# Kernel optimization log

Hardware: AMD Instinct MI355X
Metric: run time of the kernel (lower is better)

The kernel has to match this reference:

```python
import jax, jax.numpy as jnp
import numpy as np

N_NODES = 100000
N_EDGES = 1600000
IN_F = 128
HID = 64
N_CLASSES = 2


def gcn_conv(x, W, b, src, dst, dinv, n):
    # x: [N, Fin]; W: [Fin, Fout]; src/dst: [E'] (with self-loops); dinv: [N]
    h = x @ W                                    # [N, Fout]
    norm = dinv[src] * dinv[dst]                 # [E'] symmetric normalization
    msg = h[src] * norm[:, None]                 # gather + scale, [E', Fout]
    out = jax.ops.segment_sum(msg, dst, num_segments=n)  # scatter-add, [N, Fout]
    return out + b


def setup_inputs() -> dict:
    key = jax.random.key(0)
    k1, k2, k3, k4 = jax.random.split(key, 4)
    x = jax.random.normal(k1, (N_NODES, IN_F), dtype=jnp.float32)
    edge_index = jax.random.randint(k2, (2, N_EDGES), 0, N_NODES, dtype=jnp.int64)
    W1 = jax.random.normal(k3, (IN_F, HID), dtype=jnp.float32) * (1.0 / np.sqrt(IN_F))
    b1 = jnp.zeros((HID,), dtype=jnp.float32)
    W2 = jax.random.normal(k4, (HID, N_CLASSES), dtype=jnp.float32) * (1.0 / np.sqrt(HID))
    b2 = jnp.zeros((N_CLASSES,), dtype=jnp.float32)
    return {"x": x, "edge_index": edge_index, "W1": W1, "b1": b1, "W2": W2, "b2": b2}


def reference(x, edge_index, W1, b1, W2, b2):
    n = x.shape[0]
    # add self-loops (PyG GCNConv default add_self_loops=True)
    loops = jnp.arange(n, dtype=edge_index.dtype)
    src = jnp.concatenate([edge_index[0], loops])
    dst = jnp.concatenate([edge_index[1], loops])
    # degrees on dst (with self-loops) -> D^{-1/2}; deg >= 1 so no div-by-zero
    deg = jax.ops.segment_sum(jnp.ones_like(dst, dtype=x.dtype), dst, num_segments=n)
    dinv = jax.lax.rsqrt(deg)
    h = gcn_conv(x, W1, b1, src, dst, dinv, n)
    h = jax.nn.relu(h)
    # dropout p=0.5 only in training mode; reference runs eval -> identity
    out = gcn_conv(h, W2, b2, src, dst, dinv, n)
    return out
```

## Files before the change

kernel.cpp:

```cpp
#include <hip/hip_runtime.h>
#include <hip/hip_fp16.h>

#define N_NODES 100000
#define N_EDGES 1600000
#define IN_F 128
#define HID 64
#define NBUCK 1563
#define NBP 1600
#define GS 512

typedef _Float16 half8 __attribute__((ext_vector_type(8)));
typedef _Float16 half4v __attribute__((ext_vector_type(4)));
typedef _Float16 half2v __attribute__((ext_vector_type(2)));
typedef float f32x4 __attribute__((ext_vector_type(4)));

__global__ __launch_bounds__(256) void k_hist_g(const int* __restrict__ dst,
                                                unsigned short* __restrict__ gcnt) {
    __shared__ int h[NBP];
    for (int t = threadIdx.x; t < NBP; t += 256) h[t] = 0;
    __syncthreads();
    const int g = blockIdx.x;
    const int NQ = N_EDGES / 4;
    const int4* dst4 = (const int4*)dst;
    for (int q = g * 256 + threadIdx.x; q < NQ; q += GS * 256) {
        int4 d4 = dst4[q];
        atomicAdd(&h[d4.x >> 6], 1);
        atomicAdd(&h[d4.y >> 6], 1);
        atomicAdd(&h[d4.z >> 6], 1);
        atomicAdd(&h[d4.w >> 6], 1);
    }
    __syncthreads();
    unsigned int* row = (unsigned int*)(gcnt + g * NBP);
    for (int t = threadIdx.x; t < NBP / 2; t += 256)
        row[t] = (unsigned)h[2 * t] | ((unsigned)h[2 * t + 1] << 16);
}

__global__ __launch_bounds__(512) void k_gbase(const unsigned short* __restrict__ gcnt,
                                               unsigned short* __restrict__ pre,
                                               int* __restrict__ bt) {
    __shared__ uint4 s[512];
    const int t = threadIdx.x;
    const int b0 = blockIdx.x * 8;
    const int g = ((t & 63) << 3) | (t >> 6);
    uint4 v = *(const uint4*)(gcnt + g * NBP + b0);
    uint4 run = v;
    s[t] = run;
    __syncthreads();
    for (int o = 1; o < 512; o <<= 1) {
        uint4 tt = {0u, 0u, 0u, 0u};
        if (t >= o) tt = s[t - o];
        __syncthreads();
        run.x += tt.x; run.y += tt.y; run.z += tt.z; run.w += tt.w;
        s[t] = run;
        __syncthreads();
    }
    uint4 ex = { run.x - v.x, run.y - v.y, run.z - v.z, run.w - v.w };
    *(uint4*)(pre + g * NBP + b0) = ex;
    if (t == 511) {
        bt[b0 + 0] = run.x & 0xFFFF; bt[b0 + 1] = run.x >> 16;
        bt[b0 + 2] = run.y & 0xFFFF; bt[b0 + 3] = run.y >> 16;
        bt[b0 + 4] = run.z & 0xFFFF; bt[b0 + 5] = run.z >> 16;
        bt[b0 + 6] = run.w & 0xFFFF; bt[b0 + 7] = run.w >> 16;
    }
}

__global__ __launch_bounds__(1024) void k_bscan(const int* __restrict__ bt,
                                                int* __restrict__ bbase,
                                                int* __restrict__ off) {
    __shared__ int s[1024];
    const int t = threadIdx.x;
    int v0 = (2 * t < 1568) ? bt[2 * t] : 0;
    int v1 = (2 * t + 1 < 1568) ? bt[2 * t + 1] : 0;
    int p = v0 + v1;
    s[t] = p;
    __syncthreads();
    for (int o = 1; o < 1024; o <<= 1) {
        int tt = (t >= o) ? s[t - o] : 0;
        __syncthreads();
        s[t] += tt;
        __syncthreads();
    }
    int base = s[t] - p;
    bbase[2 * t] = base;
    bbase[2 * t + 1] = base + v0;
    if (t == 0) off[N_NODES] = N_EDGES;
}

__global__ __launch_bounds__(256) void k_bin(const int* __restrict__ src,
                                             const int* __restrict__ dst,
                                             const int* __restrict__ bbase,
                                             const unsigned short* __restrict__ pre,
                                             int* __restrict__ bin) {
    __shared__ int cur[NBP];
    const int g = blockIdx.x;
    const unsigned short* prow = pre + g * NBP;
    for (int t = threadIdx.x; t < NBP; t += 256)
        cur[t] = (t < NBUCK) ? (bbase[t] + (int)prow[t]) : 0;
    __syncthreads();
    const int NQ = N_EDGES / 4;
    const int4* src4 = (const int4*)src;
    const int4* dst4 = (const int4*)dst;
    for (int q = g * 256 + threadIdx.x; q < NQ; q += GS * 256) {
        int4 s4 = src4[q];
        int4 d4 = dst4[q];
        int slot;
        slot = atomicAdd(&cur[d4.x >> 6], 1); bin[slot] = ((d4.x & 63) << 17) | s4.x;
        slot = atomicAdd(&cur[d4.y >> 6], 1); bin[slot] = ((d4.y & 63) << 17) | s4.y;
        slot = atomicAdd(&cur[d4.z >> 6], 1); bin[slot] = ((d4.z & 63) << 17) | s4.z;
        slot = atomicAdd(&cur[d4.w >> 6], 1); bin[slot] = ((d4.w & 63) << 17) | s4.w;
    }
}

__global__ __launch_bounds__(256) void k_csr(const int* __restrict__ bin,
                                             const int* __restrict__ bbase,
                                             int* __restrict__ off,
                                             float* __restrict__ dinv,
                                             int* __restrict__ csr) {
    __shared__ int cnt64[64];
    __shared__ int cur64[64];
    const int b = blockIdx.x;
    if (threadIdx.x < 64) cnt64[threadIdx.x] = 0;
    __syncthreads();
    const int beg = bbase[b], end = bbase[b + 1];
    for (int i = beg + threadIdx.x; i < end; i += 256)
        atomicAdd(&cnt64[(bin[i] >> 17) & 63], 1);
    __syncthreads();
    if (threadIdx.x == 0) {
        int run = beg;
        #pragma unroll
        for (int j = 0; j < 64; ++j) {
            cur64[j] = run;
            run += cnt64[j];
        }
    }
    __syncthreads();
    if (threadIdx.x < 64) {
        int node = b * 64 + threadIdx.x;
        if (node < N_NODES) {
            off[node] = cur64[threadIdx.x];
            dinv[node] = rsqrtf((float)(cnt64[threadIdx.x] + 1));
        }
    }
    __syncthreads();
    for (int i = beg + threadIdx.x; i < end; i += 256) {
        int v = bin[i];
        int slot = atomicAdd(&cur64[(v >> 17) & 63], 1);
        csr[slot] = v & 0x1FFFF;
    }
}

__global__ __launch_bounds__(256) void k_gemm1(const float* __restrict__ x,
                                               const float* __restrict__ W1,
                                               const float* __restrict__ dinv,
                                               __half* __restrict__ hout) {
    __shared__ _Float16 Wl[8192];
    const int tid = threadIdx.x, wave = tid >> 6, lane = tid & 63;
    const int quad = lane >> 4, m = lane & 15;
    if (blockIdx.x == 0 && tid < 32) ((int*)hout)[(size_t)N_NODES * 32 + tid] = 0;
    for (int it = 0; it < 16; ++it) {
        int p = it * 256 + tid;
        int j2 = p & 3, ln = (p >> 2) & 63, kc = (p >> 8) & 3, nt = p >> 10;
        int k = kc * 32 + ((ln >> 4) << 3) + j2 * 2;
        int n = nt * 16 + (ln & 15);
        Wl[p * 2]     = (_Float16)W1[k * HID + n];
        Wl[p * 2 + 1] = (_Float16)W1[(k + 1) * HID + n];
    }
    __syncthreads();
    half8 bf[16];
    #pragma unroll
    for (int i = 0; i < 16; ++i) bf[i] = ((const half8*)Wl)[i * 64 + lane];

    const int ngroups = NBUCK;
    for (int g = blockIdx.x; g < ngroups; g += gridDim.x) {
        const int n0 = g * 64 + wave * 16;
        if (n0 >= N_NODES) continue;
        const float4* xrow = (const float4*)(x + (size_t)(n0 + m) * IN_F);
        f32x4 acc[4] = {{0.f,0.f,0.f,0.f},{0.f,0.f,0.f,0.f},
                        {0.f,0.f,0.f,0.f},{0.f,0.f,0.f,0.f}};
        #pragma unroll
        for (int kc = 0; kc < 4; ++kc) {
            float4 p0 = xrow[kc * 8 + quad * 2 + 0];
            float4 p1 = xrow[kc * 8 + quad * 2 + 1];
            half8 a;
            a[0] = (_Float16)p0.x; a[1] = (_Float16)p0.y;
            a[2] = (_Float16)p0.z; a[3] = (_Float16)p0.w;
            a[4] = (_Float16)p1.x; a[5] = (_Float16)p1.y;
            a[6] = (_Float16)p1.z; a[7] = (_Float16)p1.w;
            #pragma unroll
            for (int nt = 0; nt < 4; ++nt)
                acc[nt] = __builtin_amdgcn_mfma_f32_16x16x32_f16(a, bf[nt * 4 + kc], acc[nt], 0, 0, 0);
        }
        float di[4];
        #pragma unroll
        for (int r = 0; r < 4; ++r) di[r] = dinv[n0 + quad * 4 + r];
        _Float16* hp = (_Float16*)hout;
        #pragma unroll
        for (int nt = 0; nt < 4; ++nt)
            #pragma unroll
            for (int r = 0; r < 4; ++r)
                hp[(size_t)(n0 + quad * 4 + r) * HID + nt * 16 + m] =
                    (_Float16)(acc[nt][r] * di[r]);
    }
}

__global__ __launch_bounds__(256) void k_gather1(const __half* __restrict__ h1,
                                                 const int* __restrict__ off,
                                                 const int* __restrict__ csr,
                                                 const float* __restrict__ dinv,
                                                 const float* __restrict__ b1,
                                                 const float* __restrict__ W2,
                                                 float2* __restrict__ h2p) {
    const int wave = threadIdx.x >> 6, lane = threadIdx.x & 63;
    const int grp = lane >> 4, fl = lane & 15;
    const int d = blockIdx.x * 4 + wave;
    if (d > N_NODES) return;
    if (d == N_NODES) {
        if (lane == 0) h2p[d] = make_float2(0.f, 0.f);
        return;
    }
    const int beg = off[d], end = off[d + 1];
    const half4v* hrows = (const half4v*)h1;
    float a0 = 0.f, a1 = 0.f, a2 = 0.f, a3 = 0.f;
    for (int base = beg; base < end; base += 64) {
        const int cnt = min(64, end - base);
        int sidx = (lane < cnt) ? csr[base + lane] : N_NODES;
        for (int j = 0; j < cnt; j += 16) {
            int ss[4];
            #pragma unroll
            for (int u = 0; u < 4; ++u)
                ss[u] = __shfl(sidx, (j + 4 * u + grp) & 63, 64);
            half4v v[4];
            #pragma unroll
            for (int u = 0; u < 4; ++u)
                v[u] = hrows[(size_t)ss[u] * 16 + fl];
            half2v p0 = {(_Float16)0.f, (_Float16)0.f};
            half2v p1 = {(_Float16)0.f, (_Float16)0.f};
            #pragma unroll
            for (int u = 0; u < 4; ++u) {
                p0 += __builtin_shufflevector(v[u], v[u], 0, 1);
                p1 += __builtin_shufflevector(v[u], v[u], 2, 3);
            }
            a0 += (float)p0[0]; a1 += (float)p0[1];
            a2 += (float)p1[0]; a3 += (float)p1[1];
        }
    }
    #pragma unroll
    for (int o = 32; o >= 16; o >>= 1) {
        a0 += __shfl_xor(a0, o, 64);
        a1 += __shfl_xor(a1, o, 64);
        a2 += __shfl_xor(a2, o, 64);
        a3 += __shfl_xor(a3, o, 64);
    }
    half4v sv = hrows[(size_t)d * 16 + fl];
    a0 += (float)sv[0]; a1 += (float)sv[1]; a2 += (float)sv[2]; a3 += (float)sv[3];
    const float di = dinv[d];
    float4 bb = ((const float4*)b1)[fl];
    float y0 = fmaxf(di * a0 + bb.x, 0.f);
    float y1 = fmaxf(di * a1 + bb.y, 0.f);
    float y2 = fmaxf(di * a2 + bb.z, 0.f);
    float y3 = fmaxf(di * a3 + bb.w, 0.f);
    float4 w01 = ((const float4*)W2)[2 * fl];
    float4 w23 = ((const float4*)W2)[2 * fl + 1];
    float c0 = y0 * w01.x + y1 * w01.z + y2 * w23.x + y3 * w23.z;
    float c1 = y0 * w01.y + y1 * w01.w + y2 * w23.y + y3 * w23.w;
    #pragma unroll
    for (int o = 8; o > 0; o >>= 1) {
        c0 += __shfl_xor(c0, o, 64);
        c1 += __shfl_xor(c1, o, 64);
    }
    if (lane == 0) h2p[d] = make_float2(c0 * di, c1 * di);
}

__global__ __launch_bounds__(256) void k_gather2(const float2* __restrict__ h2p,
                                                 const int* __restrict__ off,
                                                 const int* __restrict__ csr,
                                                 const float* __restrict__ dinv,
                                                 const float* __restrict__ b2,
                                                 float* __restrict__ out) {
    int i = blockIdx.x * 256 + threadIdx.x;
    if (i >= N_NODES) return;
    int beg = off[i], end = off[i + 1];
    float2 a = h2p[i];
    for (int s = beg; s < end; s += 4) {
        int node[4];
        #pragma unroll
        for (int u = 0; u < 4; ++u) {
            int idx = s + u;
            int n = csr[min(idx, end - 1)];
            node[u] = (idx < end) ? n : N_NODES;
        }
        float2 v[4];
        #pragma unroll
        for (int u = 0; u < 4; ++u) v[u] = h2p[node[u]];
        #pragma unroll
        for (int u = 0; u < 4; ++u) { a.x += v[u].x; a.y += v[u].y; }
    }
    float di = dinv[i];
    float2 o2 = make_float2(di * a.x + b2[0], di * a.y + b2[1]);
    ((float2*)out)[i] = o2;
}

extern "C" void kernel_launch(void* const* d_in, const int* in_sizes, int n_in,
                              void* d_out, int out_size, void* d_ws, size_t ws_size,
                              hipStream_t stream) {
    const float* x  = (const float*)d_in[0];
    const int*   ei = (const int*)d_in[1];
    const float* W1 = (const float*)d_in[2];
    const float* b1 = (const float*)d_in[3];
    const float* W2 = (const float*)d_in[4];
    const float* b2 = (const float*)d_in[5];
    float* out = (float*)d_out;

    const int* src = ei;
    const int* dst = ei + N_EDGES;

    int*            wsi   = (int*)d_ws;
    unsigned short* gcnt  = (unsigned short*)wsi;
    unsigned short* pre   = (unsigned short*)(wsi + 409600);
    int*            bt    = wsi + 819200;
    int*            bbase = wsi + 821248;
    int*            off   = wsi + 823296;
    float*          dinv  = (float*)(wsi + 923648);
    int*            bin   = wsi + 1024000;
    int*            csr   = wsi + 2624000;
    __half*         h1p   = (__half*)(wsi + 4224000);
    float2*         h2p   = (float2*)(wsi + 7424064);

    dim3 B(256);
    k_hist_g <<<GS, B, 0, stream>>>(dst, gcnt);
    k_gbase  <<<196, 512, 0, stream>>>(gcnt, pre, bt);
    k_bscan  <<<1, 1024, 0, stream>>>(bt, bbase, off);
    k_bin    <<<GS, B, 0, stream>>>(src, dst, bbase, pre, bin);
    k_csr    <<<NBUCK, B, 0, stream>>>(bin, bbase, off, dinv, csr);

    k_gemm1  <<<512, B, 0, stream>>>(x, W1, dinv, h1p);
    k_gather1<<<N_NODES / 4 + 1, B, 0, stream>>>(h1p, off, csr, dinv, b1, W2, h2p);
    k_gather2<<<(N_NODES + 255) / 256, B, 0, stream>>>(h2p, off, csr, dinv, b2, out);
}
```

Before: 191.2 us.

## Split layer-1 aggregation into slice-parallel gather and separate layer-2 projection kernel

Replaces the fused gather1 kernel (one wave per node, 8-byte loads per lane) with k_aggy, where each 16-lane group handles one node and one 16-byte feature slice, with edges strided across lanes and the sums combined by a shuffle reduction. It then writes the ReLU'd hidden activations to a new fp16 buffer. A second kernel, k_gemm2y, applies W2 from shared memory and scales by dinv. The aim is wider vector loads and more parallelism per node. In exchange, every CSR index is read once per slice (8 times per edge) and an extra 12.8 MB intermediate is written and read back.

```diff
diff --git a/kernel.cpp b/kernel.cpp
--- a/kernel.cpp
+++ b/kernel.cpp
@@ -10,8 +10,6 @@
 #define GS 512
 
 typedef _Float16 half8 __attribute__((ext_vector_type(8)));
-typedef _Float16 half4v __attribute__((ext_vector_type(4)));
-typedef _Float16 half2v __attribute__((ext_vector_type(2)));
 typedef float f32x4 __attribute__((ext_vector_type(4)));
 
 __global__ __launch_bounds__(256) void k_hist_g(const int* __restrict__ dst,
@@ -203,72 +201,76 @@
     }
 }
 
-__global__ __launch_bounds__(256) void k_gather1(const __half* __restrict__ h1,
-                                                 const int* __restrict__ off,
-                                                 const int* __restrict__ csr,
-                                                 const float* __restrict__ dinv,
-                                                 const float* __restrict__ b1,
-                                                 const float* __restrict__ W2,
-                                                 float2* __restrict__ h2p) {
-    const int wave = threadIdx.x >> 6, lane = threadIdx.x & 63;
-    const int grp = lane >> 4, fl = lane & 15;
-    const int d = blockIdx.x * 4 + wave;
-    if (d > N_NODES) return;
-    if (d == N_NODES) {
-        if (lane == 0) h2p[d] = make_float2(0.f, 0.f);
-        return;
-    }
+__global__ __launch_bounds__(256) void k_aggy(const __half* __restrict__ h1,
+                                              const int* __restrict__ off,
+                                              const int* __restrict__ csr,
+                                              const float* __restrict__ dinv,
+                                              const float* __restrict__ b1,
+                                              __half* __restrict__ y) {
+    const int tid = threadIdx.x, wave = tid >> 6, lane = tid & 63;
+    const int g = lane >> 4, l = lane & 15;
+    const int s = blockIdx.x & 7;
+    const int nb = blockIdx.x >> 3;
+    const int d = nb * 16 + wave * 4 + g;
     const int beg = off[d], end = off[d + 1];
-    const half4v* hrows = (const half4v*)h1;
-    float a0 = 0.f, a1 = 0.f, a2 = 0.f, a3 = 0.f;
-    for (int base = beg; base < end; base += 64) {
-        const int cnt = min(64, end - base);
-        int sidx = (lane < cnt) ? csr[base + lane] : N_NODES;
-        for (int j = 0; j < cnt; j += 16) {
-            int ss[4];
-            #pragma unroll
-            for (int u = 0; u < 4; ++u)
-                ss[u] = __shfl(sidx, (j + 4 * u + grp) & 63, 64);
-            half4v v[4];
-            #pragma unroll
-            for (int u = 0; u < 4; ++u)
-                v[u] = hrows[(size_t)ss[u] * 16 + fl];
-            half2v p0 = {(_Float16)0.f, (_Float16)0.f};
-            half2v p1 = {(_Float16)0.f, (_Float16)0.f};
-            #pragma unroll
-            for (int u = 0; u < 4; ++u) {
-                p0 += __builtin_shufflevector(v[u], v[u], 0, 1);
-                p1 += __builtin_shufflevector(v[u], v[u], 2, 3);
-            }
-            a0 += (float)p0[0]; a1 += (float)p0[1];
-            a2 += (float)p1[0]; a3 += (float)p1[1];
-        }
-    }
-    #pragma unroll
-    for (int o = 32; o >= 16; o >>= 1) {
-        a0 += __shfl_xor(a0, o, 64);
-        a1 += __shfl_xor(a1, o, 64);
-        a2 += __shfl_xor(a2, o, 64);
-        a3 += __shfl_xor(a3, o, 64);
-    }
-    half4v sv = hrows[(size_t)d * 16 + fl];
-    a0 += (float)sv[0]; a1 += (float)sv[1]; a2 += (float)sv[2]; a3 += (float)sv[3];
-    const float di = dinv[d];
-    float4 bb = ((const float4*)b1)[fl];
-    float y0 = fmaxf(di * a0 + bb.x, 0.f);
-    float y1 = fmaxf(di * a1 + bb.y, 0.f);
-    float y2 = fmaxf(di * a2 + bb.z, 0.f);
-    float y3 = fmaxf(di * a3 + bb.w, 0.f);
-    float4 w01 = ((const float4*)W2)[2 * fl];
-    float4 w23 = ((const float4*)W2)[2 * fl + 1];
-    float c0 = y0 * w01.x + y1 * w01.z + y2 * w23.x + y3 * w23.z;
-    float c1 = y0 * w01.y + y1 * w01.w + y2 * w23.y + y3 * w23.w;
+    const half8* rows = (const half8*)h1;
+    half8 acc;
+    #pragma unroll
+    for (int i = 0; i < 8; ++i) acc[i] = (_Float16)0.f;
+    for (int p = beg + l; p < end; p += 16) {
+        int sr = csr[p];
+        acc += rows[(size_t)sr * 8 + s];
+    }
+    float f[8];
+    #pragma unroll
+    for (int i = 0; i < 8; ++i) f[i] = (float)acc[i];
     #pragma unroll
     for (int o = 8; o > 0; o >>= 1) {
-        c0 += __shfl_xor(c0, o, 64);
-        c1 += __shfl_xor(c1, o, 64);
-    }
-    if (lane == 0) h2p[d] = make_float2(c0 * di, c1 * di);
+        #pragma unroll
+        for (int i = 0; i < 8; ++i) f[i] += __shfl_xor(f[i], o, 64);
+    }
+    if (l == 0) {
+        half8 sv = rows[(size_t)d * 8 + s];
+        float di = dinv[d];
+        float4 ba = ((const float4*)b1)[s * 2];
+        float4 bb = ((const float4*)b1)[s * 2 + 1];
+        half8 outv;
+        outv[0] = (_Float16)fmaxf(di * (f[0] + (float)sv[0]) + ba.x, 0.f);
+        outv[1] = (_Float16)fmaxf(di * (f[1] + (float)sv[1]) + ba.y, 0.f);
+        outv[2] = (_Float16)fmaxf(di * (f[2] + (float)sv[2]) + ba.z, 0.f);
+        outv[3] = (_Float16)fmaxf(di * (f[3] + (float)sv[3]) + ba.w, 0.f);
+        outv[4] = (_Float16)fmaxf(di * (f[4] + (float)sv[4]) + bb.x, 0.f);
+        outv[5] = (_Float16)fmaxf(di * (f[5] + (float)sv[5]) + bb.y, 0.f);
+        outv[6] = (_Float16)fmaxf(di * (f[6] + (float)sv[6]) + bb.z, 0.f);
+        outv[7] = (_Float16)fmaxf(di * (f[7] + (float)sv[7]) + bb.w, 0.f);
+        ((half8*)y)[(size_t)d * 8 + s] = outv;
+    }
+}
+
+__global__ __launch_bounds__(256) void k_gemm2y(const __half* __restrict__ y,
+                                                const float* __restrict__ W2,
+                                                const float* __restrict__ dinv,
+                                                float2* __restrict__ h2p) {
+    __shared__ float Ws[HID * 2];
+    if (threadIdx.x < HID * 2) Ws[threadIdx.x] = W2[threadIdx.x];
+    __syncthreads();
+    int i = blockIdx.x * 256 + threadIdx.x;
+    if (i > N_NODES) return;
+    if (i == N_NODES) { h2p[i] = make_float2(0.f, 0.f); return; }
+    const half8* yr = (const half8*)y + (size_t)i * 8;
+    float c0 = 0.f, c1 = 0.f;
+    #pragma unroll
+    for (int q = 0; q < 8; ++q) {
+        half8 v = yr[q];
+        #pragma unroll
+        for (int j = 0; j < 8; ++j) {
+            float vf = (float)v[j];
+            c0 += vf * Ws[(q * 8 + j) * 2];
+            c1 += vf * Ws[(q * 8 + j) * 2 + 1];
+        }
+    }
+    float di = dinv[i];
+    h2p[i] = make_float2(c0 * di, c1 * di);
 }
 
 __global__ __launch_bounds__(256) void k_gather2(const float2* __restrict__ h2p,
@@ -325,6 +327,7 @@
     int*            csr   = wsi + 2624000;
     __half*         h1p   = (__half*)(wsi + 4224000);
     float2*         h2p   = (float2*)(wsi + 7424064);
+    __half*         yb    = (__half*)(wsi + 7624192);
 
     dim3 B(256);
     k_hist_g <<<GS, B, 0, stream>>>(dst, gcnt);
@@ -334,6 +337,7 @@
     k_csr    <<<NBUCK, B, 0, stream>>>(bin, bbase, off, dinv, csr);
 
     k_gemm1  <<<512, B, 0, stream>>>(x, W1, dinv, h1p);
-    k_gather1<<<N_NODES / 4 + 1, B, 0, stream>>>(h1p, off, csr, dinv, b1, W2, h2p);
+    k_aggy   <<<50000, B, 0, stream>>>(h1p, off, csr, dinv, b1, yb);
+    k_gemm2y <<<392, B, 0, stream>>>(yb, W2, dinv, h2p);
     k_gather2<<<(N_NODES + 255) / 256, B, 0, stream>>>(h2p, off, csr, dinv, b2, out);
 }
```

After: 335.8 us. +75.6%, slower.
